# Kernel optimization log

Measured on AMD Instinct MI355X. Metric: run time of the kernel, lower is better.

Reference implementation:

```python
import jax, jax.numpy as jnp
import numpy as np

N_NODES = 50000
N_EDGES = 600000
N_GRAPHS = 256
D = 128          # hidden_dim
L = 4            # num_layer
OUT = 1          # output_dim
ATOM_DIMS = [119, 5, 12, 12, 10, 6, 6, 2, 2]   # table size = dim+1, pad to 120
BOND_DIMS = [6, 6, 2, 2, 2]                    # table size = dim+1, pad to 7
BN_EPS = 1e-5


def setup_inputs() -> dict:
    key = jax.random.key(0)
    ks = jax.random.split(key, 16)
    x = jax.random.randint(ks[0], (N_NODES, 9), 0, 3)
    edge_index = jax.random.randint(ks[1], (2, N_EDGES), 0, N_NODES)
    edge_attr = jax.random.randint(ks[2], (N_EDGES, 5), 0, 3)
    batch = jnp.sort(jax.random.randint(ks[3], (N_NODES,), 0, N_GRAPHS))
    s = 0.1
    # padded atom embedding tables: [9, 120, D] (rows beyond dim+1 unused)
    atom_emb = jax.random.normal(ks[4], (9, 120, D), jnp.float32) * s
    # padded bond tables per layer: [L, 5, 7, D]
    bond_emb = jax.random.normal(ks[5], (L, 5, 7, D), jnp.float32) * s
    lin_w = jax.random.normal(ks[6], (L, D, D), jnp.float32) * (1.0 / np.sqrt(D))
    lin_b = jnp.zeros((L, D), jnp.float32)
    bn_gamma = jnp.ones((L, D), jnp.float32)
    bn_beta = jnp.zeros((L, D), jnp.float32)
    mlp_w1 = jax.random.normal(ks[7], (D // 2, D), jnp.float32) * (1.0 / np.sqrt(D))
    mlp_b1 = jnp.zeros((D // 2,), jnp.float32)
    mlp_w2 = jax.random.normal(ks[8], (OUT, D // 2), jnp.float32) * (1.0 / np.sqrt(D // 2))
    mlp_b2 = jnp.zeros((OUT,), jnp.float32)
    return dict(x=x, edge_index=edge_index, edge_attr=edge_attr, batch=batch,
                atom_emb=atom_emb, bond_emb=bond_emb, lin_w=lin_w, lin_b=lin_b,
                bn_gamma=bn_gamma, bn_beta=bn_beta,
                mlp_w1=mlp_w1, mlp_b1=mlp_b1, mlp_w2=mlp_w2, mlp_b2=mlp_b2)


def _multi_embed(tables, idx):
    # tables: [F, V, D], idx: [N, F] -> sum_f tables[f][idx[:, f]]
    return jax.vmap(lambda t, i: t[i], in_axes=(0, 1))(tables, idx).sum(0)


def reference(x, edge_index, edge_attr, batch, atom_emb, bond_emb, lin_w, lin_b,
              bn_gamma, bn_beta, mlp_w1, mlp_b1, mlp_w2, mlp_b2):
    n = x.shape[0]
    loop = jnp.arange(n, dtype=edge_index.dtype)
    src = jnp.concatenate([edge_index[0], loop])           # x_j (source)
    dst = jnp.concatenate([edge_index[1], loop])           # aggregate into target i
    ea = jnp.concatenate([edge_attr, jnp.zeros((n, 5), edge_attr.dtype)], axis=0)
    h = _multi_embed(atom_emb, x)                          # [N, D]
    for l in range(L):
        e_emb = _multi_embed(bond_emb[l], ea)              # [E+N, D]
        msg = h[src] + e_emb                               # gather + add
        aggr = jax.ops.segment_sum(msg, dst, num_segments=n)
        z = aggr @ lin_w[l].T + lin_b[l]
        mu = z.mean(0)
        var = z.var(0)                                     # biased, matches torch BN fwd
        h = jax.nn.relu((z - mu) * jax.lax.rsqrt(var + BN_EPS) * bn_gamma[l] + bn_beta[l])
    # global mean pool
    sums = jax.ops.segment_sum(h, batch, num_segments=N_GRAPHS)
    cnt = jax.ops.segment_sum(jnp.ones((n,), h.dtype), batch, num_segments=N_GRAPHS)
    g = sums / jnp.maximum(cnt, 1.0)[:, None]
    # MLP head (dropout inactive at inference)
    out = jax.nn.relu(g @ mlp_w1.T + mlp_b1) @ mlp_w2.T + mlp_b2
    return out
```

## Files before the change

kernel.cpp:

```cpp
#include <hip/hip_runtime.h>
#include <hip/hip_bf16.h>
#include <stdint.h>

#define D 128
#define NGRAPH 256
#define BN_EPS 1e-5f
#define NCOMBO 243
#define AGG_BLOCKS 512
#define AGG_THREADS 768
#define MAXDEG 48
#define GEMM_ROWS 128

typedef unsigned short u16;
typedef __attribute__((ext_vector_type(8))) short bf16x8;
typedef __attribute__((ext_vector_type(4))) float f32x4;

__device__ inline u16 f2bf(float a) {
  return __builtin_bit_cast(u16, __float2bfloat16(a));
}
__device__ inline uint32_t pk2(float a, float b) {
  return (uint32_t)f2bf(a) | ((uint32_t)f2bf(b) << 16);
}
__device__ inline float bflo(uint32_t u) { return __builtin_bit_cast(float, u << 16); }
__device__ inline float bfhi(uint32_t u) { return __builtin_bit_cast(float, u & 0xffff0000u); }
__device__ inline float bf1(u16 u) { return __builtin_bit_cast(float, (uint32_t)u << 16); }
__device__ inline void unpack8(uint4 v, float* f) {
  f[0] = bflo(v.x); f[1] = bfhi(v.x); f[2] = bflo(v.y); f[3] = bfhi(v.y);
  f[4] = bflo(v.z); f[5] = bfhi(v.z); f[6] = bflo(v.w); f[7] = bfhi(v.w);
}

__global__ __launch_bounds__(256) void setup_kernel(
    const int* __restrict__ x, const float* __restrict__ atom_emb,
    u16* __restrict__ h0,
    const int* __restrict__ src, const int* __restrict__ dst,
    const int* __restrict__ attr, int* __restrict__ deg,
    uint32_t* __restrict__ edges, int ne,
    const int* __restrict__ batch, int* __restrict__ goff,
    float* __restrict__ gsum, int n) {
  int b = blockIdx.x, tid = threadIdx.x;
  int nscat = (ne + 255) >> 8;
  int nemb = (n * 32 + 255) >> 8;
  if (b < nscat) {
    int e = b * 256 + tid;
    if (e >= ne) return;
    int d = dst[e];
    int slot = atomicAdd(&deg[d], 1);
    if (slot >= MAXDEG) return;
    int a0 = attr[e * 5 + 0], a1 = attr[e * 5 + 1], a2 = attr[e * 5 + 2];
    int a3 = attr[e * 5 + 3], a4 = attr[e * 5 + 4];
    uint32_t combo = (uint32_t)(a0 * 81 + a1 * 27 + a2 * 9 + a3 * 3 + a4);
    edges[(size_t)d * MAXDEG + slot] = (uint32_t)src[e] | (combo << 16);
  } else if (b < nscat + nemb) {
    int t = (b - nscat) * 256 + tid;
    int node = t >> 5, cq = t & 31;
    if (node >= n) return;
    float4 acc = {0.f, 0.f, 0.f, 0.f};
#pragma unroll
    for (int f = 0; f < 9; f++) {
      int idx = x[node * 9 + f];
      const float4* row = (const float4*)(atom_emb + ((size_t)f * 120 + idx) * D);
      float4 v = row[cq];
      acc.x += v.x; acc.y += v.y; acc.z += v.z; acc.w += v.w;
    }
    uint2 o = {pk2(acc.x, acc.y), pk2(acc.z, acc.w)};
    ((uint2*)(h0 + (size_t)node * D))[cq] = o;
  } else {
    if (b == nscat + nemb) {
      for (int t = tid; t < 4 * 2 * D; t += 256) gsum[t] = 0.f;
    }
    int i = (b - nscat - nemb) * 256 + tid;
    if (i >= n) return;
    int bb = batch[i];
    if (i == 0) {
      for (int g = 0; g <= bb; g++) goff[g] = 0;
    } else {
      int pb = batch[i - 1];
      for (int g = pb + 1; g <= bb; g++) goff[g] = i;
    }
    if (i == n - 1) {
      for (int g = bb + 1; g <= NGRAPH; g++) goff[g] = n;
    }
  }
}

__global__ __launch_bounds__(128) void prep_kernel(
    const float* __restrict__ bemb, const float* __restrict__ linw,
    u16* __restrict__ tabB, u16* __restrict__ wball) {
  __shared__ float row[D];
  int b = blockIdx.x, c = threadIdx.x;
  if (b < 4 * NCOMBO) {
    int l = b / NCOMBO, r = b % NCOMBO;
    const float* bond = bemb + (size_t)l * 5 * 7 * D;
    const float* W = linw + (size_t)l * D * D;
    int a0 = r / 81, a1 = (r / 27) % 3, a2 = (r / 9) % 3, a3 = (r / 3) % 3,
        a4 = r % 3;
    float v = bond[(0 * 7 + a0) * D + c] + bond[(1 * 7 + a1) * D + c] +
              bond[(2 * 7 + a2) * D + c] + bond[(3 * 7 + a3) * D + c] +
              bond[(4 * 7 + a4) * D + c];
    row[c] = v;
    __syncthreads();
    float s = 0.f;
    for (int k = 0; k < D; k++) s += row[k] * W[(size_t)c * D + k];
    tabB[((size_t)l * NCOMBO + r) * D + c] = f2bf(s);
  } else {
    int i = b - 4 * NCOMBO;
    int l = i >> 7, j = i & 127;
    float v = linw[(size_t)l * D * D + (size_t)j * D + c];
    wball[(size_t)l * D * D + (size_t)j * D + (c ^ ((j & 7) << 3))] = f2bf(v);
  }
}

__global__ __launch_bounds__(256) void gemm_kernel(const u16* __restrict__ in,
                                                   const u16* __restrict__ Wb,
                                                   const float* __restrict__ gsum,
                                                   const float* __restrict__ gamma,
                                                   const float* __restrict__ beta,
                                                   float invN,
                                                   u16* __restrict__ out, int M) {
  __shared__ u16 wlds[D * D];
  __shared__ float bns[2 * D];
  int tid = threadIdx.x;
  for (int i = tid; i < D * D / 8; i += 256)
    ((uint4*)wlds)[i] = ((const uint4*)Wb)[i];
  if (gsum && tid < D) {
    float s = gsum[tid], q = gsum[D + tid];
    float mu = s * invN;
    float var = q * invN - mu * mu;
    float sc = rsqrtf(var + BN_EPS) * gamma[tid];
    bns[tid] = sc;
    bns[D + tid] = beta[tid] - mu * sc;
  }
  __syncthreads();

  int wave = tid >> 6, lane = tid & 63;
  int quad = lane >> 4, l16 = lane & 15;
  int m0 = blockIdx.x * GEMM_ROWS + wave * 32;

  f32x4 acc[2][8];
#pragma unroll
  for (int mt = 0; mt < 2; mt++)
#pragma unroll
    for (int t = 0; t < 8; t++) acc[mt][t] = (f32x4){0.f, 0.f, 0.f, 0.f};

#pragma unroll
  for (int kk = 0; kk < 4; kk++) {
    int k0 = kk * 32 + quad * 8;
    bf16x8 a[2];
#pragma unroll
    for (int mt = 0; mt < 2; mt++) {
      int m = m0 + mt * 16 + l16;
      if (m < M) {
        uint4 v = *(const uint4*)(in + (size_t)m * D + k0);
        if (gsum) {
          float f[8];
          unpack8(v, f);
          float4 sc0 = *(const float4*)(bns + k0);
          float4 sc1 = *(const float4*)(bns + k0 + 4);
          float4 sh0 = *(const float4*)(bns + D + k0);
          float4 sh1 = *(const float4*)(bns + D + k0 + 4);
          f[0] = fmaxf(f[0] * sc0.x + sh0.x, 0.f);
          f[1] = fmaxf(f[1] * sc0.y + sh0.y, 0.f);
          f[2] = fmaxf(f[2] * sc0.z + sh0.z, 0.f);
          f[3] = fmaxf(f[3] * sc0.w + sh0.w, 0.f);
          f[4] = fmaxf(f[4] * sc1.x + sh1.x, 0.f);
          f[5] = fmaxf(f[5] * sc1.y + sh1.y, 0.f);
          f[6] = fmaxf(f[6] * sc1.z + sh1.z, 0.f);
          f[7] = fmaxf(f[7] * sc1.w + sh1.w, 0.f);
          v = (uint4){pk2(f[0], f[1]), pk2(f[2], f[3]),
                      pk2(f[4], f[5]), pk2(f[6], f[7])};
        }
        a[mt] = __builtin_bit_cast(bf16x8, v);
      } else {
        uint4 pz = {0u, 0u, 0u, 0u};
        a[mt] = __builtin_bit_cast(bf16x8, pz);
      }
    }
#pragma unroll
    for (int nt = 0; nt < 8; nt++) {
      int nrow = nt * 16 + l16;
      uint4 braw = *(const uint4*)(wlds + nrow * D + (k0 ^ ((nrow & 7) << 3)));
      bf16x8 bfrag = __builtin_bit_cast(bf16x8, braw);
      acc[0][nt] = __builtin_amdgcn_mfma_f32_16x16x32_bf16(a[0], bfrag, acc[0][nt], 0, 0, 0);
      acc[1][nt] = __builtin_amdgcn_mfma_f32_16x16x32_bf16(a[1], bfrag, acc[1][nt], 0, 0, 0);
    }
  }
#pragma unroll
  for (int mt = 0; mt < 2; mt++)
#pragma unroll
    for (int r = 0; r < 4; r++) {
      int row = m0 + mt * 16 + quad * 4 + r;
      if (row < M) {
#pragma unroll
        for (int nt = 0; nt < 8; nt++)
          out[(size_t)row * D + nt * 16 + l16] = f2bf(acc[mt][nt][r]);
      }
    }
}

__global__ __launch_bounds__(AGG_THREADS, 6) void agg_kernel(
    const u16* __restrict__ ht, const u16* __restrict__ tabT,
    const float* __restrict__ linb, const uint32_t* __restrict__ edges,
    const int* __restrict__ deg, u16* __restrict__ z,
    float* __restrict__ gsum, int n) {
  __shared__ u16 tabs[NCOMBO * D];
  __shared__ float psum[2 * D];
  int tid = threadIdx.x;
  for (int i = tid; i < NCOMBO * D / 8; i += AGG_THREADS)
    ((uint4*)tabs)[i] = ((const uint4*)tabT)[i];
  if (tid < 2 * D) psum[tid] = 0.f;
  __syncthreads();

  int lane = tid & 63;
  int g = lane >> 4;
  int c8 = lane & 15;
  int wid = (blockIdx.x * AGG_THREADS + tid) >> 6;
  int nw = (gridDim.x * AGG_THREADS) >> 6;

  float lbz[8];
  {
    float4 l0 = ((const float4*)linb)[c8 * 2];
    float4 l1 = ((const float4*)linb)[c8 * 2 + 1];
    float t0[8];
    unpack8(*(const uint4*)(tabs + c8 * 8), t0);
    lbz[0] = l0.x + t0[0]; lbz[1] = l0.y + t0[1];
    lbz[2] = l0.z + t0[2]; lbz[3] = l0.w + t0[3];
    lbz[4] = l1.x + t0[4]; lbz[5] = l1.y + t0[5];
    lbz[6] = l1.z + t0[6]; lbz[7] = l1.w + t0[7];
  }
  float st[8];
#pragma unroll
  for (int i = 0; i < 8; i++) st[i] = 0.f;

  int dgv = (wid < n) ? deg[wid] : 0;
  for (int node = wid; node < n; node += nw) {
    int dg = dgv;
    if (node + nw < n) dgv = deg[node + nw];
    int cnt = (dg > MAXDEG) ? MAXDEG : dg;
    int base = node * MAXDEG;
    int e = base + cnt;
    int j = base + g;

    uint4 selfv;
    if (g == 0) selfv = *(const uint4*)(ht + (size_t)node * D + c8 * 8);
    bool v0 = j < e, v1 = j + 4 < e, v2 = j + 8 < e;
    uint32_t rA, rB, rC;
    if (v0) rA = edges[j];
    if (v1) rB = edges[j + 4];
    if (v2) rC = edges[j + 8];
    uint4 hA, hB;
    if (v0) hA = *(const uint4*)(ht + (size_t)(rA & 0xffffu) * D + c8 * 8);
    if (v1) hB = *(const uint4*)(ht + (size_t)(rB & 0xffffu) * D + c8 * 8);

    float acc[8];
#pragma unroll
    for (int i = 0; i < 8; i++) acc[i] = 0.f;

    while (v0) {
      bool v3 = j + 12 < e;
      uint32_t rN;
      if (v3) rN = edges[j + 12];
      uint4 hC;
      if (v2) hC = *(const uint4*)(ht + (size_t)(rC & 0xffffu) * D + c8 * 8);
      uint4 tb = *(const uint4*)(tabs + (size_t)(rA >> 16) * D + c8 * 8);
      float hf[8], tf[8];
      unpack8(hA, hf);
      unpack8(tb, tf);
#pragma unroll
      for (int i = 0; i < 8; i++) acc[i] += hf[i] + tf[i];
      rA = rB; rB = rC; rC = rN;
      hA = hB; hB = hC;
      v0 = v1; v1 = v2; v2 = v3;
      j += 4;
    }

    if (g == 0) {
      float sv[8];
      unpack8(selfv, sv);
#pragma unroll
      for (int i = 0; i < 8; i++) acc[i] += sv[i] + lbz[i];
    }

#pragma unroll
    for (int off = 16; off <= 32; off <<= 1)
#pragma unroll
      for (int i = 0; i < 8; i++) acc[i] += __shfl_xor(acc[i], off, 64);

    if (g == 0) {
      uint4 zo = {pk2(acc[0], acc[1]), pk2(acc[2], acc[3]),
                  pk2(acc[4], acc[5]), pk2(acc[6], acc[7])};
      *(uint4*)(z + (size_t)node * D + c8 * 8) = zo;
    } else if (g == 1) {
#pragma unroll
      for (int i = 0; i < 8; i++) st[i] += acc[i];
    } else if (g == 2) {
#pragma unroll
      for (int i = 0; i < 8; i++) st[i] += acc[i] * acc[i];
    }
  }
  {
    int c0 = c8 * 8;
    if (g == 1) {
#pragma unroll
      for (int i = 0; i < 8; i++) atomicAdd(&psum[c0 + i], st[i]);
    } else if (g == 2) {
#pragma unroll
      for (int i = 0; i < 8; i++) atomicAdd(&psum[D + c0 + i], st[i]);
    }
  }
  __syncthreads();
  if (tid < 2 * D) atomicAdd(&gsum[tid], psum[tid]);
}

__global__ __launch_bounds__(512) void poolmlp_kernel(
    const u16* __restrict__ z, const float* __restrict__ gsum,
    const float* __restrict__ gamma, const float* __restrict__ beta,
    float invN, const int* __restrict__ goff,
    const float* __restrict__ w1, const float* __restrict__ b1,
    const float* __restrict__ w2, const float* __restrict__ b2,
    float* __restrict__ out) {
  __shared__ float sdata[512];
  __shared__ float pg[D];
  int g = blockIdx.x;
  int c = threadIdx.x & 127, r4 = threadIdx.x >> 7;
  float s0 = gsum[c], q0 = gsum[D + c];
  float mu = s0 * invN;
  float var = q0 * invN - mu * mu;
  float sc = rsqrtf(var + BN_EPS) * gamma[c];
  float sh = beta[c] - mu * sc;
  int s = goff[g], cnt = goff[g + 1] - s;
  float acc = 0.f;
  for (int i = r4; i < cnt; i += 4) {
    float zv = bf1(z[(size_t)(s + i) * D + c]);
    acc += fmaxf(zv * sc + sh, 0.f);
  }
  sdata[threadIdx.x] = acc;
  __syncthreads();
  if (r4 == 0) {
    float t = sdata[c] + sdata[128 + c] + sdata[256 + c] + sdata[384 + c];
    pg[c] = t / fmaxf((float)cnt, 1.f);
  }
  __syncthreads();
  if (threadIdx.x < 64) {
    int j = threadIdx.x;
    float v = b1[j];
    for (int k = 0; k < D; k++) v += pg[k] * w1[(size_t)j * D + k];
    v = fmaxf(v, 0.f) * w2[j];
#pragma unroll
    for (int off = 32; off > 0; off >>= 1) v += __shfl_down(v, off, 64);
    if (j == 0) out[g] = v + b2[0];
  }
}

extern "C" void kernel_launch(void* const* d_in, const int* in_sizes, int n_in,
                              void* d_out, int out_size, void* d_ws, size_t ws_size,
                              hipStream_t stream) {
  const int*   x     = (const int*)d_in[0];
  const int*   eidx  = (const int*)d_in[1];
  const int*   eattr = (const int*)d_in[2];
  const int*   batch = (const int*)d_in[3];
  const float* aemb  = (const float*)d_in[4];
  const float* bemb  = (const float*)d_in[5];
  const float* linw  = (const float*)d_in[6];
  const float* linb  = (const float*)d_in[7];
  const float* gamma = (const float*)d_in[8];
  const float* beta  = (const float*)d_in[9];
  const float* w1    = (const float*)d_in[10];
  const float* b1    = (const float*)d_in[11];
  const float* w2    = (const float*)d_in[12];
  const float* b2    = (const float*)d_in[13];
  float* out = (float*)d_out;

  int n  = in_sizes[3];
  int ne = in_sizes[1] / 2;
  float invN = 1.f / (float)n;

  char* p = (char*)d_ws;
  auto alloc = [&](size_t bytes) {
    char* r = p;
    p += (bytes + 255) & ~(size_t)255;
    return r;
  };
  u16*      bufA   = (u16*)alloc((size_t)n * D * 2);
  u16*      bufB   = (u16*)alloc((size_t)n * D * 2);
  uint32_t* edges  = (uint32_t*)alloc((size_t)n * MAXDEG * 4);
  int*      deg    = (int*)alloc((size_t)n * 4);
  int*      goff   = (int*)alloc((size_t)(NGRAPH + 1) * 4);
  u16*      tabB   = (u16*)alloc((size_t)4 * NCOMBO * D * 2);
  u16*      wball  = (u16*)alloc((size_t)4 * D * D * 2);
  float*    gsum   = (float*)alloc((size_t)4 * 2 * D * 4);

  hipMemsetAsync(deg, 0, (size_t)n * 4, stream);

  int nscat = (ne + 255) >> 8;
  int nemb = (n * 32 + 255) >> 8;
  int ngoff = (n + 255) >> 8;
  setup_kernel<<<nscat + nemb + ngoff, 256, 0, stream>>>(
      x, aemb, bufA, eidx, eidx + ne, eattr, deg, edges, ne, batch, goff,
      gsum, n);
  prep_kernel<<<4 * NCOMBO + 4 * D, 128, 0, stream>>>(bemb, linw, tabB, wball);

  for (int l = 0; l < 4; l++) {
    gemm_kernel<<<(n + GEMM_ROWS - 1) / GEMM_ROWS, 256, 0, stream>>>(
        bufA, wball + (size_t)l * D * D,
        l ? (gsum + (size_t)(l - 1) * 2 * D) : (const float*)nullptr,
        l ? (gamma + (size_t)(l - 1) * D) : (const float*)nullptr,
        l ? (beta + (size_t)(l - 1) * D) : (const float*)nullptr,
        invN, bufB, n);
    agg_kernel<<<AGG_BLOCKS, AGG_THREADS, 0, stream>>>(
        bufB, tabB + (size_t)l * NCOMBO * D, linb + (size_t)l * D, edges, deg,
        bufA, gsum + (size_t)l * 2 * D, n);
  }
  poolmlp_kernel<<<NGRAPH, 512, 0, stream>>>(
      bufA, gsum + 3 * 2 * D, gamma + 3 * D, beta + 3 * D, invN, goff,
      w1, b1, w2, b2, out);
}
```

Before: 376.3 us.

## Drop LDS weight staging in GEMM, read weights from global with smaller row tiles

The GEMM kernel no longer copies the 32KB bf16 weight matrix into shared memory. Instead each wave reads its B fragments straight from global memory, relying on L2/cache reuse. The weight swizzle is removed to match, and the per-block BN scale/shift precompute is replaced by each lane recomputing mean, variance and rsqrt inline from global gsum, gamma and beta. Each wave now handles 16 rows instead of 32 (64 rows per block), giving more blocks and less per-block setup, at the cost of more global weight traffic and redundant BN arithmetic.

Result: slower. 427.7 us (+13.7%).

```diff
diff --git a/kernel.cpp b/kernel.cpp
--- a/kernel.cpp
+++ b/kernel.cpp
@@ -9,7 +9,7 @@
 #define AGG_BLOCKS 512
 #define AGG_THREADS 768
 #define MAXDEG 48
-#define GEMM_ROWS 128
+#define GEMM_ROWS 64
 
 typedef unsigned short u16;
 typedef __attribute__((ext_vector_type(8))) short bf16x8;
@@ -106,7 +106,7 @@
     int i = b - 4 * NCOMBO;
     int l = i >> 7, j = i & 127;
     float v = linw[(size_t)l * D * D + (size_t)j * D + c];
-    wball[(size_t)l * D * D + (size_t)j * D + (c ^ ((j & 7) << 3))] = f2bf(v);
+    wball[(size_t)l * D * D + (size_t)j * D + c] = f2bf(v);
   }
 }
 
@@ -117,84 +117,74 @@
                                                    const float* __restrict__ beta,
                                                    float invN,
                                                    u16* __restrict__ out, int M) {
-  __shared__ u16 wlds[D * D];
-  __shared__ float bns[2 * D];
   int tid = threadIdx.x;
-  for (int i = tid; i < D * D / 8; i += 256)
-    ((uint4*)wlds)[i] = ((const uint4*)Wb)[i];
-  if (gsum && tid < D) {
-    float s = gsum[tid], q = gsum[D + tid];
-    float mu = s * invN;
-    float var = q * invN - mu * mu;
-    float sc = rsqrtf(var + BN_EPS) * gamma[tid];
-    bns[tid] = sc;
-    bns[D + tid] = beta[tid] - mu * sc;
-  }
-  __syncthreads();
-
   int wave = tid >> 6, lane = tid & 63;
   int quad = lane >> 4, l16 = lane & 15;
-  int m0 = blockIdx.x * GEMM_ROWS + wave * 32;
-
-  f32x4 acc[2][8];
-#pragma unroll
-  for (int mt = 0; mt < 2; mt++)
-#pragma unroll
-    for (int t = 0; t < 8; t++) acc[mt][t] = (f32x4){0.f, 0.f, 0.f, 0.f};
+  int m0 = blockIdx.x * GEMM_ROWS + wave * 16;
+  int m = m0 + l16;
+  bool valid = m < M;
+
+  f32x4 acc[8];
+#pragma unroll
+  for (int t = 0; t < 8; t++) acc[t] = (f32x4){0.f, 0.f, 0.f, 0.f};
 
 #pragma unroll
   for (int kk = 0; kk < 4; kk++) {
     int k0 = kk * 32 + quad * 8;
-    bf16x8 a[2];
-#pragma unroll
-    for (int mt = 0; mt < 2; mt++) {
-      int m = m0 + mt * 16 + l16;
-      if (m < M) {
-        uint4 v = *(const uint4*)(in + (size_t)m * D + k0);
-        if (gsum) {
-          float f[8];
-          unpack8(v, f);
-          float4 sc0 = *(const float4*)(bns + k0);
-          float4 sc1 = *(const float4*)(bns + k0 + 4);
-          float4 sh0 = *(const float4*)(bns + D + k0);
-          float4 sh1 = *(const float4*)(bns + D + k0 + 4);
-          f[0] = fmaxf(f[0] * sc0.x + sh0.x, 0.f);
-          f[1] = fmaxf(f[1] * sc0.y + sh0.y, 0.f);
-          f[2] = fmaxf(f[2] * sc0.z + sh0.z, 0.f);
-          f[3] = fmaxf(f[3] * sc0.w + sh0.w, 0.f);
-          f[4] = fmaxf(f[4] * sc1.x + sh1.x, 0.f);
-          f[5] = fmaxf(f[5] * sc1.y + sh1.y, 0.f);
-          f[6] = fmaxf(f[6] * sc1.z + sh1.z, 0.f);
-          f[7] = fmaxf(f[7] * sc1.w + sh1.w, 0.f);
-          v = (uint4){pk2(f[0], f[1]), pk2(f[2], f[3]),
-                      pk2(f[4], f[5]), pk2(f[6], f[7])};
-        }
-        a[mt] = __builtin_bit_cast(bf16x8, v);
-      } else {
-        uint4 pz = {0u, 0u, 0u, 0u};
-        a[mt] = __builtin_bit_cast(bf16x8, pz);
+    bf16x8 a;
+    if (valid) {
+      uint4 v = *(const uint4*)(in + (size_t)m * D + k0);
+      if (gsum) {
+        float f[8];
+        unpack8(v, f);
+        float4 s0 = *(const float4*)(gsum + k0);
+        float4 s1 = *(const float4*)(gsum + k0 + 4);
+        float4 q0 = *(const float4*)(gsum + D + k0);
+        float4 q1 = *(const float4*)(gsum + D + k0 + 4);
+        float4 g0 = *(const float4*)(gamma + k0);
+        float4 g1 = *(const float4*)(gamma + k0 + 4);
+        float4 b0 = *(const float4*)(beta + k0);
+        float4 b1 = *(const float4*)(beta + k0 + 4);
+        float mu, var, sc;
+#define BNAPP(i, S, Q, G, B)                                   \
+        mu = (S) * invN;                                       \
+        var = (Q) * invN - mu * mu;                            \
+        sc = rsqrtf(var + BN_EPS) * (G);                       \
+        f[i] = fmaxf(f[i] * sc + ((B) - mu * sc), 0.f);
+        BNAPP(0, s0.x, q0.x, g0.x, b0.x)
+        BNAPP(1, s0.y, q0.y, g0.y, b0.y)
+        BNAPP(2, s0.z, q0.z, g0.z, b0.z)
+        BNAPP(3, s0.w, q0.w, g0.w, b0.w)
+        BNAPP(4, s1.x, q1.x, g1.x, b1.x)
+        BNAPP(5, s1.y, q1.y, g1.y, b1.y)
+        BNAPP(6, s1.z, q1.z, g1.z, b1.z)
+        BNAPP(7, s1.w, q1.w, g1.w, b1.w)
+#undef BNAPP
+        v = (uint4){pk2(f[0], f[1]), pk2(f[2], f[3]),
+                    pk2(f[4], f[5]), pk2(f[6], f[7])};
       }
+      a = __builtin_bit_cast(bf16x8, v);
+    } else {
+      uint4 pz = {0u, 0u, 0u, 0u};
+      a = __builtin_bit_cast(bf16x8, pz);
     }
 #pragma unroll
     for (int nt = 0; nt < 8; nt++) {
       int nrow = nt * 16 + l16;
-      uint4 braw = *(const uint4*)(wlds + nrow * D + (k0 ^ ((nrow & 7) << 3)));
+      uint4 braw = *(const uint4*)(Wb + (size_t)nrow * D + k0);
       bf16x8 bfrag = __builtin_bit_cast(bf16x8, braw);
-      acc[0][nt] = __builtin_amdgcn_mfma_f32_16x16x32_bf16(a[0], bfrag, acc[0][nt], 0, 0, 0);
-      acc[1][nt] = __builtin_amdgcn_mfma_f32_16x16x32_bf16(a[1], bfrag, acc[1][nt], 0, 0, 0);
-    }
-  }
-#pragma unroll
-  for (int mt = 0; mt < 2; mt++)
-#pragma unroll
-    for (int r = 0; r < 4; r++) {
-      int row = m0 + mt * 16 + quad * 4 + r;
-      if (row < M) {
-#pragma unroll
-        for (int nt = 0; nt < 8; nt++)
-          out[(size_t)row * D + nt * 16 + l16] = f2bf(acc[mt][nt][r]);
-      }
-    }
+      acc[nt] = __builtin_amdgcn_mfma_f32_16x16x32_bf16(a, bfrag, acc[nt], 0, 0, 0);
+    }
+  }
+#pragma unroll
+  for (int r = 0; r < 4; r++) {
+    int row = m0 + quad * 4 + r;
+    if (row < M) {
+#pragma unroll
+      for (int nt = 0; nt < 8; nt++)
+        out[(size_t)row * D + nt * 16 + l16] = f2bf(acc[nt][r]);
+    }
+  }
 }
 
 __global__ __launch_bounds__(AGG_THREADS, 6) void agg_kernel(
```
